# Kernel tuning notes

Measured on AMD Instinct MI355X. Metric: run time of the kernel, lower is better.

Reference implementation:

```python
import jax, jax.numpy as jnp
import numpy as np

B, C, Hh, Ww = 4, 128, 256, 256
NH = 4          # num_heads
DK = C // NH    # 32
PH = PW = 8     # patchsize[log2(4)] = (8,8) for every head


def setup_inputs() -> dict:
    key = jax.random.key(0)
    ks = jax.random.split(key, 12)
    s = 0.02
    return {
        "x": jax.random.normal(ks[0], (B, C, Hh, Ww), jnp.float32),
        "m": jax.random.uniform(ks[1], (B, 1, Hh, Ww), jnp.float32),
        "wq": jax.random.normal(ks[2], (C, C), jnp.float32) * s,
        "bq": jnp.zeros((C,), jnp.float32),
        "wk": jax.random.normal(ks[3], (C, C), jnp.float32) * s,
        "bk": jnp.zeros((C,), jnp.float32),
        "wv": jax.random.normal(ks[4], (C, C), jnp.float32) * s,
        "bv": jnp.zeros((C,), jnp.float32),
        "wo": jax.random.normal(ks[5], (C, C, 3, 3), jnp.float32) * s,
        "bo": jnp.zeros((C,), jnp.float32),
    }


def _conv1x1(x, w, b):
    # x: [b,c,h,w], w: [o,c]
    return jnp.einsum('bchw,oc->bohw', x, w) + b[None, :, None, None]


def _to_windows(t, b, oh, ow):
    # [b,NH,DK,h,w] -> [b,NH,oh*ow, DK*PH*PW]  (matches torch permute(0,2,4,1,3,5))
    t = t.reshape(b, NH, DK, oh, PH, ow, PW)
    t = t.transpose(0, 1, 3, 5, 2, 4, 6)
    return t.reshape(b, NH, oh * ow, DK * PH * PW)


def reference(x, m, wq, bq, wk, bk, wv, bv, wo, bo):
    b, c, h, w = x.shape
    oh, ow = h // PH, w // PW
    q = _conv1x1(x, wq, bq).reshape(b, NH, DK, h, w)
    k = _conv1x1(x, wk, bk).reshape(b, NH, DK, h, w)
    v = _conv1x1(x, wv, bv).reshape(b, NH, DK, h, w)
    qw = _to_windows(q, b, oh, ow)  # [b,NH,nw,d]
    kw = _to_windows(k, b, oh, ow)
    vw = _to_windows(v, b, oh, ow)
    d = qw.shape[-1]
    # NOTE: original torch calls scores.masked_fill(m, -1e9) without assignment,
    # so the mask is a no-op; we faithfully omit it from the math.
    scores = jnp.einsum('bhnd,bhmd->bhnm', qw, kw) / jnp.sqrt(jnp.float32(d))
    p = jax.nn.softmax(scores, axis=-1)
    y = jnp.einsum('bhnm,bhmd->bhnd', p, vw)
    # inverse window partition -> [b, C, h, w] (head chunks concat along channel)
    y = y.reshape(b, NH, oh, ow, DK, PH, PW)
    y = y.transpose(0, 1, 4, 2, 5, 3, 6).reshape(b, c, h, w)
    # output: 3x3 conv with reflect padding, then LeakyReLU(0.2)
    yp = jnp.pad(y, ((0, 0), (0, 0), (1, 1), (1, 1)), mode='reflect')
    out = jax.lax.conv_general_dilated(
        yp, wo, window_strides=(1, 1), padding='VALID',
        dimension_numbers=('NCHW', 'OIHW', 'NCHW'))
    out = out + bo[None, :, None, None]
    return jnp.where(out > 0, out, 0.2 * out)
```

## Files before the change

### kernel.cpp

```cpp
#include <hip/hip_runtime.h>

typedef float f32x4 __attribute__((ext_vector_type(4)));
typedef __bf16 bf16x8 __attribute__((ext_vector_type(8)));

#define IMH 256
#define IMW 256
#define NCH 128
#define NHEAD 4
#define NWIN 1024
#define DWIN 2048
#define HW (IMH*IMW)

__device__ __forceinline__ unsigned short bf16u(float f) {
  __bf16 h = (__bf16)f;
  return __builtin_bit_cast(unsigned short, h);
}
__device__ __forceinline__ f32x4 fzero() { f32x4 z = {0.f, 0.f, 0.f, 0.f}; return z; }

__global__ void k_prep_w(const float* __restrict__ wq, const float* __restrict__ wk,
                         const float* __restrict__ wv, __bf16* __restrict__ wt) {
  int i = blockIdx.x * 256 + threadIdx.x;
  if (i < 16384) {
    wt[i]         = (__bf16)wq[i];
    wt[i + 16384] = (__bf16)wk[i];
    wt[i + 32768] = (__bf16)wv[i];
  }
}

__global__ void k_prep_wo(const float* __restrict__ wo, __bf16* __restrict__ wot) {
  int i = blockIdx.x * 256 + threadIdx.x;
  if (i < 9*16384) {
    int kk = i >> 14;
    int oc = i & 16383;
    wot[i] = (__bf16)wo[oc*9 + kk];
  }
}

__global__ __launch_bounds__(512)
void k_qkv(const float* __restrict__ x, const __bf16* __restrict__ wt,
           const float* __restrict__ bq, const float* __restrict__ bk,
           const float* __restrict__ bv,
           __bf16* __restrict__ qw, __bf16* __restrict__ kw, __bf16* __restrict__ vt) {
  __shared__ __align__(16) unsigned short xt[16384];
  __shared__ __align__(16) unsigned short rp[16384];
  const int bidx = blockIdx.x;
  const int half = bidx & 1, h = (bidx >> 1) & 255, b = bidx >> 9;
  const int py = h & 7, oy = h >> 3;
  const int w0 = half * 128;
  const int t = threadIdx.x;
  {
    const int w = t & 127, cg0 = (t >> 7) * 8;
    const float* xb = x + (size_t)(b*NCH)*HW + (size_t)h*IMW + w0 + w;
    #pragma unroll
    for (int c0i = 0; c0i < 4; ++c0i) {
      int c0 = cg0 + c0i*32;
      unsigned int pk[4];
      #pragma unroll
      for (int q = 0; q < 4; ++q) {
        float v0 = xb[(size_t)(c0 + 2*q)*HW];
        float v1 = xb[(size_t)(c0 + 2*q + 1)*HW];
        pk[q] = (unsigned int)bf16u(v0) | ((unsigned int)bf16u(v1) << 16);
      }
      uint4 val; val.x = pk[0]; val.y = pk[1]; val.z = pk[2]; val.w = pk[3];
      *(uint4*)((char*)xt + w*256 + ((c0*2) ^ ((w&7)<<4))) = val;
    }
  }
  __syncthreads();
  const int lane = t & 63, wid = t >> 6;
  const int wm = wid >> 2, wn = wid & 3;
  const int l15 = lane & 15, l4 = lane >> 4;
  for (int mat = 0; mat < 3; ++mat) {
    const __bf16* wmat = wt + mat*16384;
    const float* bias = (mat == 0) ? bq : ((mat == 1) ? bk : bv);
    f32x4 acc[4][2];
    #pragma unroll
    for (int i = 0; i < 4; ++i)
      #pragma unroll
      for (int j = 0; j < 2; ++j) acc[i][j] = fzero();
    #pragma unroll
    for (int kc = 0; kc < 4; ++kc) {
      bf16x8 a[4], bb[2];
      #pragma unroll
      for (int i = 0; i < 4; ++i) {
        int o = wm*64 + i*16 + l15;
        a[i] = *(const bf16x8*)(wmat + o*128 + kc*32 + l4*8);
      }
      #pragma unroll
      for (int j = 0; j < 2; ++j) {
        int wc = wn*32 + j*16 + l15;
        bb[j] = *(const bf16x8*)((const char*)xt + (wc*256 + ((kc*64 + l4*16) ^ ((wc&7)<<4))));
      }
      #pragma unroll
      for (int i = 0; i < 4; ++i)
        #pragma unroll
        for (int j = 0; j < 2; ++j)
          acc[i][j] = __builtin_amdgcn_mfma_f32_16x16x32_bf16(a[i], bb[j], acc[i][j], 0, 0, 0);
    }
    #pragma unroll
    for (int i = 0; i < 4; ++i)
      #pragma unroll
      for (int r = 0; r < 4; ++r) {
        int o = wm*64 + i*16 + l4*4 + r;
        float bi = bias[o];
        #pragma unroll
        for (int j = 0; j < 2; ++j) {
          int w = wn*32 + j*16 + l15;
          *(unsigned short*)((char*)rp + o*256 + ((w*2) ^ ((o&7)<<4))) =
              bf16u(acc[i][j][r] + bi);
        }
      }
    __syncthreads();
    if (mat < 2) {
      __bf16* dst = (mat == 0) ? qw : kw;
      const int px = t & 7, oxl = (t >> 3) & 15, nh = t >> 7;
      const int n = oy*32 + half*16 + oxl;
      unsigned short v[32];
      #pragma unroll
      for (int dk = 0; dk < 32; ++dk) {
        int o = nh*32 + dk;
        v[dk] = *(const unsigned short*)((const char*)rp + o*256 +
                  (((oxl*8 + px)*2) ^ ((o&7)<<4)));
      }
      unsigned short* dp = (unsigned short*)dst +
          ((size_t)(b*NHEAD + nh)*NWIN + n)*DWIN + py*256 + px*32;
      #pragma unroll
      for (int qq = 0; qq < 4; ++qq) {
        uint4 val;
        val.x = (unsigned int)v[qq*8+0] | ((unsigned int)v[qq*8+1] << 16);
        val.y = (unsigned int)v[qq*8+2] | ((unsigned int)v[qq*8+3] << 16);
        val.z = (unsigned int)v[qq*8+4] | ((unsigned int)v[qq*8+5] << 16);
        val.w = (unsigned int)v[qq*8+6] | ((unsigned int)v[qq*8+7] << 16);
        ((uint4*)dp)[qq] = val;
      }
    } else {
      #pragma unroll
      for (int it = 0; it < 2; ++it) {
        int u = it*512 + t;
        int px = u & 7, dk = (u >> 3) & 31, nh = u >> 8;
        int o = nh*32 + dk;
        unsigned short v[16];
        #pragma unroll
        for (int ox = 0; ox < 16; ++ox)
          v[ox] = *(const unsigned short*)((const char*)rp + o*256 +
                    (((ox*8 + px)*2) ^ ((o&7)<<4)));
        unsigned short* dp = (unsigned short*)vt +
            ((size_t)(b*NHEAD + nh)*DWIN + py*256 + px*32 + dk)*NWIN + oy*32 + half*16;
        #pragma unroll
        for (int qq = 0; qq < 2; ++qq) {
          uint4 val;
          val.x = (unsigned int)v[qq*8+0] | ((unsigned int)v[qq*8+1] << 16);
          val.y = (unsigned int)v[qq*8+2] | ((unsigned int)v[qq*8+3] << 16);
          val.z = (unsigned int)v[qq*8+4] | ((unsigned int)v[qq*8+5] << 16);
          val.w = (unsigned int)v[qq*8+6] | ((unsigned int)v[qq*8+7] << 16);
          ((uint4*)dp)[qq] = val;
        }
      }
    }
    __syncthreads();
  }
}

__device__ __forceinline__ void gemm_tile(const __bf16* __restrict__ A,
                                          const __bf16* __restrict__ B,
                                          const int lda, const int ldb, const int NT,
                                          unsigned short* Asm, unsigned short* Bsm,
                                          f32x4 (&acc)[4][4]) {
  const int t = threadIdx.x;
  const int lane = t & 63, wid = t >> 6;
  const int wm = wid >> 1, wn = wid & 1;
  const int l15 = lane & 15, l4 = lane >> 4;
  const int u0 = t, u1 = t + 256;
  const int ra0 = u0 >> 2, ca0 = u0 & 3;
  const int ra1 = u1 >> 2, ca1 = u1 & 3;
  uint4 ar0 = *(const uint4*)(A + ra0*lda + ca0*8);
  uint4 ar1 = *(const uint4*)(A + ra1*lda + ca1*8);
  uint4 br0 = *(const uint4*)(B + ra0*ldb + ca0*8);
  uint4 br1 = *(const uint4*)(B + ra1*ldb + ca1*8);
  for (int kt = 0; kt < NT; ++kt) {
    __syncthreads();
    *(uint4*)((char*)Asm + ra0*80 + ca0*16) = ar0;
    *(uint4*)((char*)Asm + ra1*80 + ca1*16) = ar1;
    *(uint4*)((char*)Bsm + ra0*80 + ca0*16) = br0;
    *(uint4*)((char*)Bsm + ra1*80 + ca1*16) = br1;
    __syncthreads();
    if (kt + 1 < NT) {
      int k0 = (kt+1)*32;
      ar0 = *(const uint4*)(A + ra0*lda + k0 + ca0*8);
      ar1 = *(const uint4*)(A + ra1*lda + k0 + ca1*8);
      br0 = *(const uint4*)(B + ra0*ldb + k0 + ca0*8);
      br1 = *(const uint4*)(B + ra1*ldb + k0 + ca1*8);
    }
    bf16x8 a[4], bb[4];
    #pragma unroll
    for (int i = 0; i < 4; ++i)
      a[i] = *(const bf16x8*)((const char*)Asm + (wm*64 + i*16 + l15)*80 + l4*16);
    #pragma unroll
    for (int j = 0; j < 4; ++j)
      bb[j] = *(const bf16x8*)((const char*)Bsm + (wn*64 + j*16 + l15)*80 + l4*16);
    #pragma unroll
    for (int i = 0; i < 4; ++i)
      #pragma unroll
      for (int j = 0; j < 4; ++j)
        acc[i][j] = __builtin_amdgcn_mfma_f32_16x16x32_bf16(a[i], bb[j], acc[i][j], 0, 0, 0);
  }
}

__global__ __launch_bounds__(256)
void k_scores(const __bf16* __restrict__ qw, const __bf16* __restrict__ kw,
              float* __restrict__ S) {
  __shared__ __align__(16) unsigned short Asm[5120], Bsm[5120];
  const int bnh = blockIdx.y;
  const int mt = blockIdx.x >> 3, nt = blockIdx.x & 7;
  const __bf16* A = qw + (size_t)bnh*NWIN*DWIN + (size_t)mt*128*DWIN;
  const __bf16* B = kw + (size_t)bnh*NWIN*DWIN + (size_t)nt*128*DWIN;
  f32x4 acc[4][4];
  #pragma unroll
  for (int i = 0; i < 4; ++i)
    #pragma unroll
    for (int j = 0; j < 4; ++j) acc[i][j] = fzero();
  gemm_tile(A, B, DWIN, DWIN, 64, Asm, Bsm, acc);
  const float scale = 0.022097086912079608f;
  const int t = threadIdx.x, lane = t & 63, wid = t >> 6;
  const int wm = wid >> 1, wn = wid & 1, l15 = lane & 15, l4 = lane >> 4;
  float* Sb = S + (size_t)bnh*NWIN*NWIN + (size_t)(mt*128)*NWIN + nt*128;
  #pragma unroll
  for (int i = 0; i < 4; ++i)
    #pragma unroll
    for (int r = 0; r < 4; ++r) {
      int row = wm*64 + i*16 + l4*4 + r;
      #pragma unroll
      for (int j = 0; j < 4; ++j) {
        int col = wn*64 + j*16 + l15;
        Sb[(size_t)row*NWIN + col] = acc[i][j][r] * scale;
      }
    }
}

__global__ __launch_bounds__(256)
void k_softmax(const float* __restrict__ S, __bf16* __restrict__ P) {
  __shared__ float red[8];
  const int row = blockIdx.x;
  const int t = threadIdx.x;
  const float4 v = ((const float4*)(S + (size_t)row*NWIN))[t];
  float m = fmaxf(fmaxf(v.x, v.y), fmaxf(v.z, v.w));
  for (int off = 1; off < 64; off <<= 1) m = fmaxf(m, __shfl_xor(m, off));
  const int wid = t >> 6, lane = t & 63;
  if (lane == 0) red[wid] = m;
  __syncthreads();
  m = fmaxf(fmaxf(red[0], red[1]), fmaxf(red[2], red[3]));
  float e0 = __expf(v.x - m), e1 = __expf(v.y - m), e2 = __expf(v.z - m), e3 = __expf(v.w - m);
  float s = e0 + e1 + e2 + e3;
  for (int off = 1; off < 64; off <<= 1) s += __shfl_xor(s, off);
  if (lane == 0) red[4 + wid] = s;
  __syncthreads();
  s = red[4] + red[5] + red[6] + red[7];
  float inv = 1.0f / s;
  ushort4 o;
  o.x = bf16u(e0*inv); o.y = bf16u(e1*inv); o.z = bf16u(e2*inv); o.w = bf16u(e3*inv);
  ((ushort4*)((unsigned short*)P + (size_t)row*NWIN))[t] = o;
}

__global__ __launch_bounds__(256)
void k_pv(const __bf16* __restrict__ P, const __bf16* __restrict__ vt,
          __bf16* __restrict__ y3) {
  __shared__ __align__(16) unsigned short Asm[5120], Bsm[5120];
  const int bnh = blockIdx.y;
  const int b = bnh >> 2, nh = bnh & 3;
  const int mt = blockIdx.x >> 4, nt = blockIdx.x & 15;
  const __bf16* A = P  + (size_t)bnh*NWIN*NWIN + (size_t)mt*128*NWIN;
  const __bf16* B = vt + (size_t)bnh*DWIN*NWIN + (size_t)nt*128*NWIN;
  f32x4 acc[4][4];
  #pragma unroll
  for (int i = 0; i < 4; ++i)
    #pragma unroll
    for (int j = 0; j < 4; ++j) acc[i][j] = fzero();
  gemm_tile(A, B, NWIN, NWIN, 32, Asm, Bsm, acc);
  const int t = threadIdx.x, lane = t & 63, wid = t >> 6;
  const int wm = wid >> 1, wn = wid & 1, l15 = lane & 15, l4 = lane >> 4;
  unsigned short* yu = (unsigned short*)y3;
  const size_t cbase = (size_t)(b*NHEAD + nh)*65536*32;
  #pragma unroll
  for (int i = 0; i < 4; ++i)
    #pragma unroll
    for (int r = 0; r < 4; ++r) {
      int n = mt*128 + wm*64 + i*16 + l4*4 + r;
      int oyy = n >> 5, oxx = n & 31;
      #pragma unroll
      for (int j = 0; j < 4; ++j) {
        int pp = nt*4 + wn*2 + (j >> 1);
        int dk = (j & 1)*16 + l15;
        int hh = oyy*8 + (pp >> 3), ww = oxx*8 + (pp & 7);
        yu[cbase + ((size_t)hh*256 + ww)*32 + dk] = bf16u(acc[i][j][r]);
      }
    }
}

__global__ __launch_bounds__(256)
void k_conv(const __bf16* __restrict__ y3, const __bf16* __restrict__ wot,
            const float* __restrict__ bo, float* __restrict__ out) {
  __shared__ __align__(16) unsigned short ylds[15840];
  const int bid = blockIdx.x;
  const int half = bid & 1, h = (bid >> 1) & 255, b = bid >> 9;
  const int w0 = half * 128;
  const int t = threadIdx.x;
  const int hm1 = (h == 0) ? 1 : h - 1;
  const int hp1 = (h == 255) ? 254 : h + 1;
  const int lane = t & 63, wid = t >> 6;
  const int wm = wid >> 1, wn = wid & 1, l15 = lane & 15, l4 = lane >> 4;
  f32x4 acc[4][4];
  #pragma unroll
  for (int i = 0; i < 4; ++i)
    #pragma unroll
    for (int j = 0; j < 4; ++j) acc[i][j] = fzero();
  const unsigned short* yu = (const unsigned short*)y3;
  for (int cc = 0; cc < 4; ++cc) {
    const size_t cbase = (size_t)(b*NHEAD + cc)*65536*32;
    __syncthreads();
    #pragma unroll
    for (int it = 0; it < 6; ++it) {
      int u = it*256 + t;
      int seg = u & 3, wl = (u >> 2) & 127, rowr = u >> 9;
      int hh = (rowr == 0) ? hm1 : ((rowr == 1) ? h : hp1);
      int gw = w0 - 1 + wl;
      gw = (gw < 0) ? 1 : ((gw > 255) ? 254 : gw);
      uint4 val = *(const uint4*)(yu + cbase + ((size_t)hh*256 + gw)*32 + seg*8);
      *(uint4*)((char*)ylds + (rowr*132 + wl)*80 + seg*16) = val;
    }
    if (t < 24) {
      int seg = t & 3, wl = 128 + ((t >> 2) & 1), rowr = t >> 3;
      int hh = (rowr == 0) ? hm1 : ((rowr == 1) ? h : hp1);
      int gw = w0 - 1 + wl;
      gw = (gw < 0) ? 1 : ((gw > 255) ? 254 : gw);
      uint4 val = *(const uint4*)(yu + cbase + ((size_t)hh*256 + gw)*32 + seg*8);
      *(uint4*)((char*)ylds + (rowr*132 + wl)*80 + seg*16) = val;
    }
    __syncthreads();
    #pragma unroll
    for (int kk = 0; kk < 9; ++kk) {
      const int ky = kk / 3, kx = kk % 3;
      bf16x8 a[4], bb[4];
      #pragma unroll
      for (int i = 0; i < 4; ++i) {
        int o = wm*64 + i*16 + l15;
        a[i] = *(const bf16x8*)(wot + ((size_t)kk*128 + o)*128 + cc*32 + l4*8);
      }
      #pragma unroll
      for (int j = 0; j < 4; ++j) {
        int px = wn*64 + j*16 + l15;
        int R = ky*132 + px + kx;
        bb[j] = *(const bf16x8*)((const char*)ylds + R*80 + l4*16);
      }
      #pragma unroll
      for (int i = 0; i < 4; ++i)
        #pragma unroll
        for (int j = 0; j < 4; ++j)
          acc[i][j] = __builtin_amdgcn_mfma_f32_16x16x32_bf16(a[i], bb[j], acc[i][j], 0, 0, 0);
    }
  }
  #pragma unroll
  for (int i = 0; i < 4; ++i)
    #pragma unroll
    for (int r = 0; r < 4; ++r) {
      int o = wm*64 + i*16 + l4*4 + r;
      float bi = bo[o];
      #pragma unroll
      for (int j = 0; j < 4; ++j) {
        int px = wn*64 + j*16 + l15;
        float v = acc[i][j][r] + bi;
        v = (v > 0.f) ? v : 0.2f * v;
        out[(size_t)((b*NCH + o)*IMH + h)*IMW + w0 + px] = v;
      }
    }
}

extern "C" void kernel_launch(void* const* d_in, const int* in_sizes, int n_in,
                              void* d_out, int out_size, void* d_ws, size_t ws_size,
                              hipStream_t stream) {
  (void)in_sizes; (void)n_in; (void)out_size; (void)ws_size;
  const float* x  = (const float*)d_in[0];
  const float* wq = (const float*)d_in[2];
  const float* bq = (const float*)d_in[3];
  const float* wk = (const float*)d_in[4];
  const float* bk = (const float*)d_in[5];
  const float* wv = (const float*)d_in[6];
  const float* bv = (const float*)d_in[7];
  const float* wo = (const float*)d_in[8];
  const float* bo = (const float*)d_in[9];
  float* out = (float*)d_out;
  char* ws = (char*)d_ws;
  __bf16* qw  = (__bf16*)(ws + 0);
  __bf16* kw  = (__bf16*)(ws + 67108864);
  __bf16* vt  = (__bf16*)(ws + 134217728);
  float*  S   = (float*)(ws + 201326592);
  __bf16* P   = (__bf16*)(ws + 0);
  __bf16* y3  = (__bf16*)(ws + 201326592);
  __bf16* wt  = (__bf16*)(ws + 201326592);
  __bf16* wot = (__bf16*)(ws + 67108864);

  k_prep_w<<<64, 256, 0, stream>>>(wq, wk, wv, wt);
  k_qkv<<<2048, 512, 0, stream>>>(x, wt, bq, bk, bv, qw, kw, vt);
  k_scores<<<dim3(64, 16), 256, 0, stream>>>(qw, kw, S);
  k_prep_wo<<<576, 256, 0, stream>>>(wo, wot);
  k_softmax<<<16384, 256, 0, stream>>>(S, P);
  k_pv<<<dim3(128, 16), 256, 0, stream>>>(P, vt, y3);
  k_conv<<<2048, 256, 0, stream>>>(y3, wot, bo, out);
}
```

Before: 588.3 us.

## Shrink QKV blocks to 64-pixel quarters and transpose staging layout for vector stores

Splits each image row into four 64-pixel blocks of 256 threads instead of two 128-pixel blocks of 512, halving shared memory per block so more blocks can be resident. The staging buffer is transposed to pixel-major with a 16-row XOR swizzle, so Q/K windows can be copied out with 16-byte LDS reads instead of 32 scalar reads. The V transpose path reads 32-bit pairs and packs two channels per read, and the final barrier is dropped after the last matrix. This changes the grid size and swizzle pattern, so bank conflicts and the coalescing of global writes may behave differently.

New measurement: 600.0 us. About the same (+2.0%).

```diff
diff --git a/kernel.cpp b/kernel.cpp
--- a/kernel.cpp
+++ b/kernel.cpp
@@ -36,20 +36,20 @@
   }
 }
 
-__global__ __launch_bounds__(512)
+__global__ __launch_bounds__(256, 5)
 void k_qkv(const float* __restrict__ x, const __bf16* __restrict__ wt,
            const float* __restrict__ bq, const float* __restrict__ bk,
            const float* __restrict__ bv,
            __bf16* __restrict__ qw, __bf16* __restrict__ kw, __bf16* __restrict__ vt) {
-  __shared__ __align__(16) unsigned short xt[16384];
-  __shared__ __align__(16) unsigned short rp[16384];
+  __shared__ __align__(16) unsigned short xt[8192];
+  __shared__ __align__(16) unsigned short rp[8192];
   const int bidx = blockIdx.x;
-  const int half = bidx & 1, h = (bidx >> 1) & 255, b = bidx >> 9;
+  const int quarter = bidx & 3, h = (bidx >> 2) & 255, b = bidx >> 10;
   const int py = h & 7, oy = h >> 3;
-  const int w0 = half * 128;
+  const int w0 = quarter * 64;
   const int t = threadIdx.x;
   {
-    const int w = t & 127, cg0 = (t >> 7) * 8;
+    const int w = t & 63, cg0 = (t >> 6) * 8;
     const float* xb = x + (size_t)(b*NCH)*HW + (size_t)h*IMW + w0 + w;
     #pragma unroll
     for (int c0i = 0; c0i < 4; ++c0i) {
@@ -67,7 +67,7 @@
   }
   __syncthreads();
   const int lane = t & 63, wid = t >> 6;
-  const int wm = wid >> 2, wn = wid & 3;
+  const int wm = wid >> 1, wn = wid & 1;
   const int l15 = lane & 15, l4 = lane >> 4;
   for (int mat = 0; mat < 3; ++mat) {
     const __bf16* wmat = wt + mat*16384;
@@ -97,66 +97,61 @@
           acc[i][j] = __builtin_amdgcn_mfma_f32_16x16x32_bf16(a[i], bb[j], acc[i][j], 0, 0, 0);
     }
     #pragma unroll
-    for (int i = 0; i < 4; ++i)
-      #pragma unroll
-      for (int r = 0; r < 4; ++r) {
-        int o = wm*64 + i*16 + l4*4 + r;
-        float bi = bias[o];
-        #pragma unroll
-        for (int j = 0; j < 2; ++j) {
-          int w = wn*32 + j*16 + l15;
-          *(unsigned short*)((char*)rp + o*256 + ((w*2) ^ ((o&7)<<4))) =
-              bf16u(acc[i][j][r] + bi);
-        }
-      }
+    for (int i = 0; i < 4; ++i) {
+      int o0 = wm*64 + i*16 + l4*4;
+      float b0 = bias[o0], b1 = bias[o0+1], b2 = bias[o0+2], b3 = bias[o0+3];
+      #pragma unroll
+      for (int j = 0; j < 2; ++j) {
+        int w = wn*32 + j*16 + l15;
+        uint2 pk;
+        pk.x = (unsigned int)bf16u(acc[i][j][0]+b0) | ((unsigned int)bf16u(acc[i][j][1]+b1) << 16);
+        pk.y = (unsigned int)bf16u(acc[i][j][2]+b2) | ((unsigned int)bf16u(acc[i][j][3]+b3) << 16);
+        *(uint2*)((char*)rp + w*256 + ((o0*2) ^ ((w&15)<<4))) = pk;
+      }
+    }
     __syncthreads();
     if (mat < 2) {
       __bf16* dst = (mat == 0) ? qw : kw;
-      const int px = t & 7, oxl = (t >> 3) & 15, nh = t >> 7;
-      const int n = oy*32 + half*16 + oxl;
-      unsigned short v[32];
-      #pragma unroll
-      for (int dk = 0; dk < 32; ++dk) {
-        int o = nh*32 + dk;
-        v[dk] = *(const unsigned short*)((const char*)rp + o*256 +
-                  (((oxl*8 + px)*2) ^ ((o&7)<<4)));
-      }
+      const int px = t & 7, oxl = (t >> 3) & 7, nh = t >> 6;
+      const int w = oxl*8 + px;
+      const int n = oy*32 + quarter*8 + oxl;
       unsigned short* dp = (unsigned short*)dst +
           ((size_t)(b*NHEAD + nh)*NWIN + n)*DWIN + py*256 + px*32;
       #pragma unroll
-      for (int qq = 0; qq < 4; ++qq) {
-        uint4 val;
-        val.x = (unsigned int)v[qq*8+0] | ((unsigned int)v[qq*8+1] << 16);
-        val.y = (unsigned int)v[qq*8+2] | ((unsigned int)v[qq*8+3] << 16);
-        val.z = (unsigned int)v[qq*8+4] | ((unsigned int)v[qq*8+5] << 16);
-        val.w = (unsigned int)v[qq*8+6] | ((unsigned int)v[qq*8+7] << 16);
-        ((uint4*)dp)[qq] = val;
+      for (int q = 0; q < 4; ++q) {
+        uint4 val = *(const uint4*)((const char*)rp + w*256 +
+                      (((nh*32 + q*8)*2) ^ ((w&15)<<4)));
+        ((uint4*)dp)[q] = val;
       }
     } else {
       #pragma unroll
       for (int it = 0; it < 2; ++it) {
-        int u = it*512 + t;
-        int px = u & 7, dk = (u >> 3) & 31, nh = u >> 8;
-        int o = nh*32 + dk;
-        unsigned short v[16];
+        int u = it*256 + t;
+        int px = u & 7, dkh = (u >> 3) & 15, nh = u >> 7;
+        int o = nh*32 + dkh*2;
+        unsigned int v32[8];
         #pragma unroll
-        for (int ox = 0; ox < 16; ++ox)
-          v[ox] = *(const unsigned short*)((const char*)rp + o*256 +
-                    (((ox*8 + px)*2) ^ ((o&7)<<4)));
-        unsigned short* dp = (unsigned short*)vt +
-            ((size_t)(b*NHEAD + nh)*DWIN + py*256 + px*32 + dk)*NWIN + oy*32 + half*16;
-        #pragma unroll
-        for (int qq = 0; qq < 2; ++qq) {
-          uint4 val;
-          val.x = (unsigned int)v[qq*8+0] | ((unsigned int)v[qq*8+1] << 16);
-          val.y = (unsigned int)v[qq*8+2] | ((unsigned int)v[qq*8+3] << 16);
-          val.z = (unsigned int)v[qq*8+4] | ((unsigned int)v[qq*8+5] << 16);
-          val.w = (unsigned int)v[qq*8+6] | ((unsigned int)v[qq*8+7] << 16);
-          ((uint4*)dp)[qq] = val;
+        for (int ox = 0; ox < 8; ++ox) {
+          int w = ox*8 + px;
+          v32[ox] = *(const unsigned int*)((const char*)rp + w*256 +
+                      ((o*2) ^ ((w&15)<<4)));
         }
-      }
-    }
-    __syncthreads();
+        uint4 lo, hi;
+        lo.x = (v32[0]&0xFFFFu) | (v32[1]<<16);
+        lo.y = (v32[2]&0xFFFFu) | (v32[3]<<16);
+        lo.z = (v32[4]&0xFFFFu) | (v32[5]<<16);
+        lo.w = (v32[6]&0xFFFFu) | (v32[7]<<16);
+        hi.x = (v32[0]>>16) | (v32[1]&0xFFFF0000u);
+        hi.y = (v32[2]>>16) | (v32[3]&0xFFFF0000u);
+        hi.z = (v32[4]>>16) | (v32[5]&0xFFFF0000u);
+        hi.w = (v32[6]>>16) | (v32[7]&0xFFFF0000u);
+        unsigned short* dpl = (unsigned short*)vt +
+            ((size_t)(b*NHEAD + nh)*DWIN + py*256 + px*32 + dkh*2)*NWIN + oy*32 + quarter*8;
+        *(uint4*)dpl = lo;
+        *(uint4*)(dpl + NWIN) = hi;
+      }
+    }
+    if (mat < 2) __syncthreads();
   }
 }
 
@@ -398,7 +393,7 @@
   __bf16* wot = (__bf16*)(ws + 67108864);
 
   k_prep_w<<<64, 256, 0, stream>>>(wq, wk, wv, wt);
-  k_qkv<<<2048, 512, 0, stream>>>(x, wt, bq, bk, bv, qw, kw, vt);
+  k_qkv<<<4096, 256, 0, stream>>>(x, wt, bq, bk, bv, qw, kw, vt);
   k_scores<<<dim3(64, 16), 256, 0, stream>>>(qw, kw, S);
   k_prep_wo<<<576, 256, 0, stream>>>(wo, wot);
   k_softmax<<<16384, 256, 0, stream>>>(S, P);
```
